# Kernel tuning notes

Hardware: AMD Instinct MI355X
Metric: run time of the kernel (lower is better)

Reference implementation:

```python
import jax, jax.numpy as jnp
import numpy as np

NEG_SLOPE = 0.2  # PyG GATConv default


def setup_inputs() -> dict:
    key = jax.random.key(0)
    k1, k2, k3, k4, k5, k6 = jax.random.split(key, 6)
    N, F_in, F_out, E = 50000, 512, 256, 400000
    x = jax.random.normal(k1, (N, F_in), dtype=jnp.float32)
    adj = jax.random.randint(k2, (2, E), 0, N, dtype=jnp.int64)  # [2, E] edge_index (src, dst)
    glorot = lambda k, shape: jax.random.uniform(
        k, shape, jnp.float32, -1.0, 1.0) * np.sqrt(6.0 / (shape[0] + shape[-1]))
    W = glorot(k3, (F_in, F_out))
    att_src = glorot(k4, (F_out,))
    att_dst = glorot(k5, (F_out,))
    bias = jnp.zeros((F_out,), dtype=jnp.float32)
    return {"x": x, "adj": adj, "W": W, "att_src": att_src, "att_dst": att_dst, "bias": bias}


def reference(x, adj, W, att_src, att_dst, bias):
    N = x.shape[0]
    # add self loops (PyG GATConv default add_self_loops=True)
    loops = jnp.arange(N, dtype=adj.dtype)
    src = jnp.concatenate([adj[0], loops])
    dst = jnp.concatenate([adj[1], loops])

    h = x @ W                          # [N, F_out] projected features
    a_src = h @ att_src                # [N] per-node source attention term
    a_dst = h @ att_dst                # [N]
    e = a_src[src] + a_dst[dst]        # [E+N] edge logits
    e = jnp.where(e > 0, e, NEG_SLOPE * e)  # leaky_relu

    # per-destination softmax over incoming edges (numerically stable)
    m = jax.ops.segment_max(e, dst, num_segments=N)
    ex = jnp.exp(e - m[dst])
    denom = jax.ops.segment_sum(ex, dst, num_segments=N)
    alpha = ex / denom[dst]            # [E+N]

    # weighted scatter-aggregate of source messages
    out = jax.ops.segment_sum(alpha[:, None] * h[src], dst, num_segments=N)
    out = out + bias
    return jax.nn.relu(out)
```

## Files before the change

kernel.cpp:

```cpp
#include <hip/hip_runtime.h>
#include <hip/hip_bf16.h>

typedef __attribute__((ext_vector_type(8))) short bf16x8;
typedef __attribute__((ext_vector_type(4))) float f32x4;
typedef unsigned short u16;

#define F_IN 512
#define F_OUT 256
#define NEG_SLOPE 0.2f

__device__ __forceinline__ float leaky(float e) { return e > 0.f ? e : NEG_SLOPE * e; }

__device__ __forceinline__ u16 f2bf(float x) {
    __hip_bfloat16 h = __float2bfloat16(x);
    return *reinterpret_cast<u16*>(&h);
}
__device__ __forceinline__ void bf2x2(unsigned p, float& a, float& b) {
    a = __uint_as_float(p << 16);
    b = __uint_as_float(p & 0xffff0000u);
}

__device__ __forceinline__ void dma16(const void* g, void* l) {
    __builtin_amdgcn_global_load_lds((const __attribute__((address_space(1))) void*)g,
                                     (__attribute__((address_space(3))) void*)l, 16, 0, 0);
}

__global__ void k_transpose(const float* __restrict__ W, u16* __restrict__ Wt,
                            float* __restrict__ aS, float* __restrict__ aD,
                            int* __restrict__ deg, int N) {
    int t = blockIdx.x * 256 + threadIdx.x;
    int k = t >> 8;
    int n = t & 255;
    Wt[n * F_IN + k] = f2bf(W[k * F_OUT + n]);
    if (t < N) {
        aS[t] = 0.f;
        aD[t] = 0.f;
        deg[t] = 0;
    }
}

__global__ __launch_bounds__(256) void k_gemm(const float* __restrict__ X,
                                              const u16* __restrict__ Wt,
                                              const float* __restrict__ att_src,
                                              const float* __restrict__ att_dst,
                                              u16* __restrict__ Hb,
                                              float* __restrict__ aS, float* __restrict__ aD,
                                              int N) {
    __shared__ float sA[2][128 * 32];
    __shared__ u16 sB[2][128 * 32];
    const int tid = threadIdx.x;
    const int wave = tid >> 6, lane = tid & 63;
    const int wm = (wave >> 1) * 64, wn = (wave & 1) * 64;
    const int tile_m = blockIdx.y * 128, tile_n = blockIdx.x * 128;

    f32x4 acc[4][4];
#pragma unroll
    for (int i = 0; i < 4; i++)
#pragma unroll
        for (int j = 0; j < 4; j++) acc[i][j] = (f32x4){0.f, 0.f, 0.f, 0.f};

    const int a_row_in = lane >> 3;
    const int a_gc = (lane & 7) ^ a_row_in;
    const int b_row_in = lane >> 2;
    const int b_gc = (lane & 3) ^ ((lane >> 3) & 3);

    const float* aG[4];
#pragma unroll
    for (int t = 0; t < 4; ++t) {
        int grow = tile_m + wave * 32 + t * 8 + a_row_in;
        if (grow >= N) grow = N - 1;
        aG[t] = &X[(size_t)grow * F_IN + a_gc * 4];
    }
    const u16* bG[2];
#pragma unroll
    for (int t = 0; t < 2; ++t) {
        int grow = tile_n + wave * 32 + t * 16 + b_row_in;
        bG[t] = &Wt[(size_t)grow * F_IN + b_gc * 8];
    }

    auto stage = [&](int kb, int buf) {
#pragma unroll
        for (int t = 0; t < 4; ++t)
            dma16(aG[t] + kb * 32, &sA[buf][(wave * 32 + t * 8) * 32]);
#pragma unroll
        for (int t = 0; t < 2; ++t)
            dma16(bG[t] + kb * 32, &sB[buf][(wave * 32 + t * 16) * 32]);
    };

    stage(0, 0);
    int cur = 0;
    const int lm = lane & 15, q = lane >> 4;

    for (int kb = 0; kb < F_IN / 32; ++kb) {
        if (kb + 1 < F_IN / 32) {
            stage(kb + 1, cur ^ 1);
            asm volatile("s_waitcnt vmcnt(6)" ::: "memory");
        } else {
            asm volatile("s_waitcnt vmcnt(0)" ::: "memory");
        }
        __builtin_amdgcn_sched_barrier(0);
        __builtin_amdgcn_s_barrier();

        bf16x8 af[4], bfr[4];
#pragma unroll
        for (int i = 0; i < 4; i++) {
            const int arow = wm + i * 16 + lm;
            const int s7 = arow & 7;
            const float4 c0 = *(const float4*)&sA[cur][arow * 32 + (((2 * q) ^ s7) << 2)];
            const float4 c1 = *(const float4*)&sA[cur][arow * 32 + (((2 * q + 1) ^ s7) << 2)];
            u16 a8[8] = {f2bf(c0.x), f2bf(c0.y), f2bf(c0.z), f2bf(c0.w),
                         f2bf(c1.x), f2bf(c1.y), f2bf(c1.z), f2bf(c1.w)};
            af[i] = *(const bf16x8*)a8;
            const int brow = wn + i * 16 + lm;
            bfr[i] = *(const bf16x8*)&sB[cur][brow * 32 + ((q ^ ((lm >> 1) & 3)) << 3)];
        }
#pragma unroll
        for (int i = 0; i < 4; i++)
#pragma unroll
            for (int j = 0; j < 4; j++)
                acc[i][j] = __builtin_amdgcn_mfma_f32_16x16x32_bf16(af[i], bfr[j], acc[i][j], 0, 0, 0);
        __builtin_amdgcn_s_barrier();
        cur ^= 1;
    }

    const int lc = lm, lr4 = q * 4;
    float vS[4], vD[4];
#pragma unroll
    for (int j = 0; j < 4; ++j) {
        int col = tile_n + wn + j * 16 + lc;
        vS[j] = att_src[col];
        vD[j] = att_dst[col];
    }
#pragma unroll
    for (int i = 0; i < 4; i++) {
#pragma unroll
        for (int r = 0; r < 4; r++) {
            int row = tile_m + wm + i * 16 + lr4 + r;
            float pS = acc[i][0][r] * vS[0] + acc[i][1][r] * vS[1] +
                       acc[i][2][r] * vS[2] + acc[i][3][r] * vS[3];
            float pD = acc[i][0][r] * vD[0] + acc[i][1][r] * vD[1] +
                       acc[i][2][r] * vD[2] + acc[i][3][r] * vD[3];
#pragma unroll
            for (int off = 1; off < 16; off <<= 1) {
                pS += __shfl_xor(pS, off);
                pD += __shfl_xor(pD, off);
            }
            if (lc == 0 && row < N) {
                atomicAdd(&aS[row], pS);
                atomicAdd(&aD[row], pD);
            }
        }
#pragma unroll
        for (int j = 0; j < 4; j++) {
#pragma unroll
            for (int r = 0; r < 4; r++) {
                int row = tile_m + wm + i * 16 + lr4 + r;
                int col = tile_n + wn + j * 16 + lc;
                if (row < N) Hb[(size_t)row * F_OUT + col] = f2bf(acc[i][j][r]);
            }
        }
    }
}

__global__ void k_deg(const int* __restrict__ dsts, int* __restrict__ deg, int E) {
    int e = blockIdx.x * 256 + threadIdx.x;
    if (e >= E) return;
    atomicAdd(&deg[dsts[e]], 1);
}

__global__ __launch_bounds__(256) void k_scan1(const int* __restrict__ deg,
                                               int* __restrict__ bsum, int N) {
    __shared__ int ws[4];
    int t = threadIdx.x;
    int i = blockIdx.x * 256 + t;
    int v = (i < N) ? deg[i] : 0;
    for (int off = 32; off; off >>= 1) v += __shfl_down(v, off);
    if ((t & 63) == 0) ws[t >> 6] = v;
    __syncthreads();
    if (t == 0) bsum[blockIdx.x] = ws[0] + ws[1] + ws[2] + ws[3];
}

__global__ __launch_bounds__(256) void k_scan2(const int* __restrict__ bsum,
                                               int* __restrict__ boff, int* __restrict__ offs,
                                               int nb, int N) {
    __shared__ int ss[256];
    int t = threadIdx.x;
    int v = (t < nb) ? bsum[t] : 0;
    ss[t] = v;
    __syncthreads();
    for (int off = 1; off < 256; off <<= 1) {
        int u = (t >= off) ? ss[t - off] : 0;
        __syncthreads();
        ss[t] += u;
        __syncthreads();
    }
    boff[t] = ss[t] - v;
    if (t == 255) offs[N] = ss[255];
}

__global__ __launch_bounds__(256) void k_scan3(const int* __restrict__ deg,
                                               const int* __restrict__ boff,
                                               int* __restrict__ offs, int* __restrict__ cur,
                                               int N) {
    __shared__ int ss[256];
    int t = threadIdx.x;
    int i = blockIdx.x * 256 + t;
    int v = (i < N) ? deg[i] : 0;
    ss[t] = v;
    __syncthreads();
    for (int off = 1; off < 256; off <<= 1) {
        int u = (t >= off) ? ss[t - off] : 0;
        __syncthreads();
        ss[t] += u;
        __syncthreads();
    }
    int ex = ss[t] - v + boff[blockIdx.x];
    if (i < N) {
        offs[i] = ex;
        cur[i] = ex;
    }
}

__global__ void k_edge_scatter(const int* __restrict__ srcs, const int* __restrict__ dsts,
                               const float* __restrict__ aS, const float* __restrict__ aD,
                               int* __restrict__ cur, int* __restrict__ csrS,
                               float* __restrict__ csrW, int E) {
    int e = blockIdx.x * 256 + threadIdx.x;
    if (e >= E) return;
    int s = srcs[e], d = dsts[e];
    float ex = __expf(leaky(aS[s] + aD[d]));
    int pos = atomicAdd(&cur[d], 1);
    csrS[pos] = s;
    csrW[pos] = ex;
}

__global__ __launch_bounds__(256) void k_aggregate(const u16* __restrict__ Hb,
                                                   const float* __restrict__ aS,
                                                   const float* __restrict__ aD,
                                                   const int* __restrict__ offs,
                                                   const int* __restrict__ csrS,
                                                   const float* __restrict__ csrW,
                                                   const float* __restrict__ bias,
                                                   float* __restrict__ out, int N) {
    int wave = threadIdx.x >> 6, lane = threadIdx.x & 63;
    int i = blockIdx.x * 4 + wave;
    if (i >= N) return;
    float sex = __expf(leaky(aS[i] + aD[i]));

    uint2 rv = *(const uint2*)&Hb[(size_t)i * F_OUT + lane * 4];
    float f0, f1, f2, f3;
    bf2x2(rv.x, f0, f1);
    bf2x2(rv.y, f2, f3);
    float4 acc = {sex * f0, sex * f1, sex * f2, sex * f3};
    float wsum = sex;

    int beg = offs[i], end = offs[i + 1];
    int k = beg;
    for (; k + 4 <= end; k += 4) {
        int s0 = csrS[k], s1 = csrS[k + 1], s2 = csrS[k + 2], s3 = csrS[k + 3];
        float w0 = csrW[k], w1 = csrW[k + 1], w2 = csrW[k + 2], w3 = csrW[k + 3];
        uint2 g0 = *(const uint2*)&Hb[(size_t)s0 * F_OUT + lane * 4];
        uint2 g1 = *(const uint2*)&Hb[(size_t)s1 * F_OUT + lane * 4];
        uint2 g2 = *(const uint2*)&Hb[(size_t)s2 * F_OUT + lane * 4];
        uint2 g3 = *(const uint2*)&Hb[(size_t)s3 * F_OUT + lane * 4];
        wsum += w0 + w1 + w2 + w3;
        bf2x2(g0.x, f0, f1); bf2x2(g0.y, f2, f3);
        acc.x += w0 * f0; acc.y += w0 * f1; acc.z += w0 * f2; acc.w += w0 * f3;
        bf2x2(g1.x, f0, f1); bf2x2(g1.y, f2, f3);
        acc.x += w1 * f0; acc.y += w1 * f1; acc.z += w1 * f2; acc.w += w1 * f3;
        bf2x2(g2.x, f0, f1); bf2x2(g2.y, f2, f3);
        acc.x += w2 * f0; acc.y += w2 * f1; acc.z += w2 * f2; acc.w += w2 * f3;
        bf2x2(g3.x, f0, f1); bf2x2(g3.y, f2, f3);
        acc.x += w3 * f0; acc.y += w3 * f1; acc.z += w3 * f2; acc.w += w3 * f3;
    }
    for (; k < end; ++k) {
        int s = csrS[k];
        float w = csrW[k];
        uint2 r = *(const uint2*)&Hb[(size_t)s * F_OUT + lane * 4];
        wsum += w;
        bf2x2(r.x, f0, f1);
        bf2x2(r.y, f2, f3);
        acc.x += w * f0;
        acc.y += w * f1;
        acc.z += w * f2;
        acc.w += w * f3;
    }
    float inv = 1.f / wsum;
    const float4 bv = *(const float4*)&bias[lane * 4];
    float4 o;
    o.x = acc.x * inv + bv.x;
    o.y = acc.y * inv + bv.y;
    o.z = acc.z * inv + bv.z;
    o.w = acc.w * inv + bv.w;
    o.x = o.x > 0.f ? o.x : 0.f;
    o.y = o.y > 0.f ? o.y : 0.f;
    o.z = o.z > 0.f ? o.z : 0.f;
    o.w = o.w > 0.f ? o.w : 0.f;
    *(float4*)&out[(size_t)i * F_OUT + lane * 4] = o;
}

extern "C" void kernel_launch(void* const* d_in, const int* in_sizes, int n_in,
                              void* d_out, int out_size, void* d_ws, size_t ws_size,
                              hipStream_t stream) {
    const float* X = (const float*)d_in[0];
    const int* adj = (const int*)d_in[1];
    const float* W = (const float*)d_in[2];
    const float* att_src = (const float*)d_in[3];
    const float* att_dst = (const float*)d_in[4];
    const float* bias = (const float*)d_in[5];
    float* out = (float*)d_out;

    const int N = in_sizes[0] / F_IN;
    const int E = in_sizes[1] / 2;
    const int* srcs = adj;
    const int* dsts = adj + E;
    const int nb = (N + 255) / 256;

    char* p = (char*)d_ws;
    auto take = [&](size_t b) -> char* {
        char* q = p;
        p += (b + 255) & ~(size_t)255;
        return q;
    };
    u16* Hb = (u16*)take((size_t)N * F_OUT * sizeof(u16));
    u16* Wt = (u16*)take((size_t)F_IN * F_OUT * sizeof(u16));
    float* aS = (float*)take((size_t)N * sizeof(float));
    float* aD = (float*)take((size_t)N * sizeof(float));
    int* deg = (int*)take((size_t)N * sizeof(int));
    int* offs = (int*)take((size_t)(N + 1) * sizeof(int));
    int* cur = (int*)take((size_t)N * sizeof(int));
    int* bsum = (int*)take((size_t)256 * sizeof(int));
    int* boff = (int*)take((size_t)256 * sizeof(int));
    int* csrS = (int*)take((size_t)E * sizeof(int));
    float* csrW = (float*)take((size_t)E * sizeof(float));

    k_transpose<<<(F_IN * F_OUT) / 256, 256, 0, stream>>>(W, Wt, aS, aD, deg, N);
    dim3 ggrid((F_OUT + 127) / 128, (N + 127) / 128);
    k_gemm<<<ggrid, 256, 0, stream>>>(X, Wt, att_src, att_dst, Hb, aS, aD, N);
    k_deg<<<(E + 255) / 256, 256, 0, stream>>>(dsts, deg, E);
    k_scan1<<<nb, 256, 0, stream>>>(deg, bsum, N);
    k_scan2<<<1, 256, 0, stream>>>(bsum, boff, offs, nb, N);
    k_scan3<<<nb, 256, 0, stream>>>(deg, boff, offs, cur, N);
    k_edge_scatter<<<(E + 255) / 256, 256, 0, stream>>>(srcs, dsts, aS, aD, cur, csrS, csrW, E);
    k_aggregate<<<(N + 3) / 4, 256, 0, stream>>>(Hb, aS, aD, offs, csrS, csrW, bias, out, N);
}
```

Baseline: 293.4 us.

## Retile GEMM to full-width 64-row blocks, loading B directly from global

The GEMM now uses 64-row tiles, each covering all 256 output columns, with each wave owning a 64-column slice. X tiles are streamed into a 4-deep LDS ring with a prefetch distance of 2, and the bf16 weight fragments are read straight from global memory (L2-resident) rather than staged through LDS. Because one block now holds whole rows, the attention dot products are reduced across waves in shared memory and written with plain stores, which removes the atomics and the zero-initialisation of aS/aD. The risks are global-load latency on B inside the k-loop and that X is read once per block, against fewer blocks overall.

After: 291.6 us. Within noise of the previous version (-0.6%).

```diff
diff --git a/kernel.cpp b/kernel.cpp
--- a/kernel.cpp
+++ b/kernel.cpp
@@ -26,17 +26,12 @@
 }
 
 __global__ void k_transpose(const float* __restrict__ W, u16* __restrict__ Wt,
-                            float* __restrict__ aS, float* __restrict__ aD,
                             int* __restrict__ deg, int N) {
     int t = blockIdx.x * 256 + threadIdx.x;
     int k = t >> 8;
     int n = t & 255;
     Wt[n * F_IN + k] = f2bf(W[k * F_OUT + n]);
-    if (t < N) {
-        aS[t] = 0.f;
-        aD[t] = 0.f;
-        deg[t] = 0;
-    }
+    if (t < N) deg[t] = 0;
 }
 
 __global__ __launch_bounds__(256) void k_gemm(const float* __restrict__ X,
@@ -46,96 +41,82 @@
                                               u16* __restrict__ Hb,
                                               float* __restrict__ aS, float* __restrict__ aD,
                                               int N) {
-    __shared__ float sA[2][128 * 32];
-    __shared__ u16 sB[2][128 * 32];
+    __shared__ float sA[4][64 * 32];
     const int tid = threadIdx.x;
     const int wave = tid >> 6, lane = tid & 63;
-    const int wm = (wave >> 1) * 64, wn = (wave & 1) * 64;
-    const int tile_m = blockIdx.y * 128, tile_n = blockIdx.x * 128;
-
-    f32x4 acc[4][4];
-#pragma unroll
-    for (int i = 0; i < 4; i++)
-#pragma unroll
-        for (int j = 0; j < 4; j++) acc[i][j] = (f32x4){0.f, 0.f, 0.f, 0.f};
+    const int tile_m = blockIdx.x * 64;
+    const int lm = lane & 15, q = lane >> 4;
 
     const int a_row_in = lane >> 3;
     const int a_gc = (lane & 7) ^ a_row_in;
-    const int b_row_in = lane >> 2;
-    const int b_gc = (lane & 3) ^ ((lane >> 3) & 3);
-
-    const float* aG[4];
-#pragma unroll
-    for (int t = 0; t < 4; ++t) {
-        int grow = tile_m + wave * 32 + t * 8 + a_row_in;
+    const float* aG[2];
+#pragma unroll
+    for (int t = 0; t < 2; ++t) {
+        int grow = tile_m + wave * 16 + t * 8 + a_row_in;
         if (grow >= N) grow = N - 1;
         aG[t] = &X[(size_t)grow * F_IN + a_gc * 4];
     }
-    const u16* bG[2];
-#pragma unroll
-    for (int t = 0; t < 2; ++t) {
-        int grow = tile_n + wave * 32 + t * 16 + b_row_in;
-        bG[t] = &Wt[(size_t)grow * F_IN + b_gc * 8];
-    }
-
-    auto stage = [&](int kb, int buf) {
-#pragma unroll
-        for (int t = 0; t < 4; ++t)
-            dma16(aG[t] + kb * 32, &sA[buf][(wave * 32 + t * 8) * 32]);
+    const u16* bP[4];
+#pragma unroll
+    for (int j = 0; j < 4; j++)
+        bP[j] = &Wt[(size_t)(wave * 64 + j * 16 + lm) * F_IN + q * 8];
+
+    f32x4 acc[4][4];
+#pragma unroll
+    for (int i = 0; i < 4; i++)
+#pragma unroll
+        for (int j = 0; j < 4; j++) acc[i][j] = (f32x4){0.f, 0.f, 0.f, 0.f};
+
+    auto dmaA = [&](int kb) {
+        const int buf = kb & 3;
 #pragma unroll
         for (int t = 0; t < 2; ++t)
-            dma16(bG[t] + kb * 32, &sB[buf][(wave * 32 + t * 16) * 32]);
+            dma16(aG[t] + kb * 32, &sA[buf][(wave * 16 + t * 8) * 32]);
     };
-
-    stage(0, 0);
-    int cur = 0;
-    const int lm = lane & 15, q = lane >> 4;
+    dmaA(0);
+    dmaA(1);
 
     for (int kb = 0; kb < F_IN / 32; ++kb) {
-        if (kb + 1 < F_IN / 32) {
-            stage(kb + 1, cur ^ 1);
-            asm volatile("s_waitcnt vmcnt(6)" ::: "memory");
-        } else {
-            asm volatile("s_waitcnt vmcnt(0)" ::: "memory");
-        }
+        bf16x8 bfr[4];
+#pragma unroll
+        for (int j = 0; j < 4; j++) bfr[j] = *(const bf16x8*)(bP[j] + kb * 32);
+        if (kb + 2 < F_IN / 32) dmaA(kb + 2);
+        asm volatile("s_waitcnt vmcnt(4)" ::: "memory");
         __builtin_amdgcn_sched_barrier(0);
         __builtin_amdgcn_s_barrier();
 
-        bf16x8 af[4], bfr[4];
+        const int buf = kb & 3;
+        bf16x8 af[4];
 #pragma unroll
         for (int i = 0; i < 4; i++) {
-            const int arow = wm + i * 16 + lm;
+            const int arow = i * 16 + lm;
             const int s7 = arow & 7;
-            const float4 c0 = *(const float4*)&sA[cur][arow * 32 + (((2 * q) ^ s7) << 2)];
-            const float4 c1 = *(const float4*)&sA[cur][arow * 32 + (((2 * q + 1) ^ s7) << 2)];
+            const float4 c0 = *(const float4*)&sA[buf][arow * 32 + (((2 * q) ^ s7) << 2)];
+            const float4 c1 = *(const float4*)&sA[buf][arow * 32 + (((2 * q + 1) ^ s7) << 2)];
             u16 a8[8] = {f2bf(c0.x), f2bf(c0.y), f2bf(c0.z), f2bf(c0.w),
                          f2bf(c1.x), f2bf(c1.y), f2bf(c1.z), f2bf(c1.w)};
             af[i] = *(const bf16x8*)a8;
-            const int brow = wn + i * 16 + lm;
-            bfr[i] = *(const bf16x8*)&sB[cur][brow * 32 + ((q ^ ((lm >> 1) & 3)) << 3)];
         }
 #pragma unroll
         for (int i = 0; i < 4; i++)
 #pragma unroll
             for (int j = 0; j < 4; j++)
                 acc[i][j] = __builtin_amdgcn_mfma_f32_16x16x32_bf16(af[i], bfr[j], acc[i][j], 0, 0, 0);
-        __builtin_amdgcn_s_barrier();
-        cur ^= 1;
-    }
-
-    const int lc = lm, lr4 = q * 4;
+    }
+    __syncthreads();
+
     float vS[4], vD[4];
 #pragma unroll
     for (int j = 0; j < 4; ++j) {
-        int col = tile_n + wn + j * 16 + lc;
+        int col = wave * 64 + j * 16 + lm;
         vS[j] = att_src[col];
         vD[j] = att_dst[col];
     }
+    float* sD = (float*)sA;
 #pragma unroll
     for (int i = 0; i < 4; i++) {
 #pragma unroll
         for (int r = 0; r < 4; r++) {
-            int row = tile_m + wm + i * 16 + lr4 + r;
             float pS = acc[i][0][r] * vS[0] + acc[i][1][r] * vS[1] +
                        acc[i][2][r] * vS[2] + acc[i][3][r] * vS[3];
             float pD = acc[i][0][r] * vD[0] + acc[i][1][r] * vD[1] +
@@ -145,21 +126,33 @@
                 pS += __shfl_xor(pS, off);
                 pD += __shfl_xor(pD, off);
             }
-            if (lc == 0 && row < N) {
-                atomicAdd(&aS[row], pS);
-                atomicAdd(&aD[row], pD);
+            if (lm == 0) {
+                int rl = i * 16 + q * 4 + r;
+                sD[rl * 8 + wave * 2 + 0] = pS;
+                sD[rl * 8 + wave * 2 + 1] = pD;
             }
         }
+    }
+    __syncthreads();
+    if (tid < 64) {
+        int row = tile_m + tid;
+        if (row < N) {
+            aS[row] = sD[tid * 8 + 0] + sD[tid * 8 + 2] + sD[tid * 8 + 4] + sD[tid * 8 + 6];
+            aD[row] = sD[tid * 8 + 1] + sD[tid * 8 + 3] + sD[tid * 8 + 5] + sD[tid * 8 + 7];
+        }
+    }
+
+#pragma unroll
+    for (int i = 0; i < 4; i++)
 #pragma unroll
         for (int j = 0; j < 4; j++) {
 #pragma unroll
             for (int r = 0; r < 4; r++) {
-                int row = tile_m + wm + i * 16 + lr4 + r;
-                int col = tile_n + wn + j * 16 + lc;
+                int row = tile_m + i * 16 + q * 4 + r;
+                int col = wave * 64 + j * 16 + lm;
                 if (row < N) Hb[(size_t)row * F_OUT + col] = f2bf(acc[i][j][r]);
             }
         }
-    }
 }
 
 __global__ void k_deg(const int* __restrict__ dsts, int* __restrict__ deg, int E) {
@@ -334,9 +327,8 @@
     int* csrS = (int*)take((size_t)E * sizeof(int));
     float* csrW = (float*)take((size_t)E * sizeof(float));
 
-    k_transpose<<<(F_IN * F_OUT) / 256, 256, 0, stream>>>(W, Wt, aS, aD, deg, N);
-    dim3 ggrid((F_OUT + 127) / 128, (N + 127) / 128);
-    k_gemm<<<ggrid, 256, 0, stream>>>(X, Wt, att_src, att_dst, Hb, aS, aD, N);
+    k_transpose<<<(F_IN * F_OUT) / 256, 256, 0, stream>>>(W, Wt, deg, N);
+    k_gemm<<<(N + 63) / 64, 256, 0, stream>>>(X, Wt, att_src, att_dst, Hb, aS, aD, N);
     k_deg<<<(E + 255) / 256, 256, 0, stream>>>(dsts, deg, E);
     k_scan1<<<nb, 256, 0, stream>>>(deg, bsum, N);
     k_scan2<<<1, 256, 0, stream>>>(bsum, boff, offs, nb, N);
```
